# Kernel tuning notes

Measured on AMD Instinct MI355X. Metric: run time of the kernel, lower is better.

The kernel has to match this reference:

```python
import jax, jax.numpy as jnp
import numpy as np

B, S, D = 4, 4096, 1024
E, K, H = 8, 2, 2048


def setup_inputs() -> dict:
    key = jax.random.key(0)
    ks = jax.random.split(key, 6)
    scale_g = 1.0 / np.sqrt(D)
    scale_1 = 1.0 / np.sqrt(D)
    scale_2 = 1.0 / np.sqrt(H)
    return {
        "x": jax.random.normal(ks[0], (B, S, D), dtype=jnp.float32),
        "Wg": jax.random.uniform(ks[1], (D, E), jnp.float32, -scale_g, scale_g),
        "W1": jax.random.uniform(ks[2], (E, D, H), jnp.float32, -scale_1, scale_1),
        "b1": jax.random.uniform(ks[3], (E, H), jnp.float32, -scale_1, scale_1),
        "W2": jax.random.uniform(ks[4], (E, H, D), jnp.float32, -scale_2, scale_2),
        "b2": jax.random.uniform(ks[5], (E, D), jnp.float32, -scale_2, scale_2),
    }


def reference(x, Wg, W1, b1, W2, b2):
    # Router: softmax gate, top-k selection, renormalized combine weights
    logits = jnp.einsum("bsd,de->bse", x, Wg)          # [B,S,E]
    probs = jax.nn.softmax(logits, axis=-1)
    topv, topi = jax.lax.top_k(probs, K)                # [B,S,K]
    cw = topv / (jnp.sum(topv, axis=-1, keepdims=True) + 1e-9)
    # Per-token weight for each expert: sum over k of one_hot(idx_k)*cw_k -> [B,S,E]
    we = jnp.sum(jax.nn.one_hot(topi, E, dtype=x.dtype) * cw[..., None], axis=-2)
    # Weighted combine of per-expert FFN outputs (loop over small fixed E)
    y = jnp.zeros_like(x)
    for e in range(E):
        h = jax.nn.relu(jnp.einsum("bsd,dh->bsh", x, W1[e]) + b1[e])
        out_e = jnp.einsum("bsh,hd->bsd", h, W2[e]) + b2[e]
        y = y + we[..., e:e + 1] * out_e
    return y
```

## Files before the change

kernel.cpp:

```cpp
#include <hip/hip_runtime.h>
#include <hip/hip_bf16.h>

#define TOK 16384
#define DIM 1024
#define HID 2048
#define NEXP 8

typedef __attribute__((ext_vector_type(4))) float f32x4;
typedef __attribute__((ext_vector_type(8))) short s16x8;

__device__ __forceinline__ unsigned short f2bf(float f) {
  union { float f; unsigned u; } v; v.f = f;
  unsigned r = v.u + 0x7fffu + ((v.u >> 16) & 1u);
  return (unsigned short)(r >> 16);
}
__device__ __forceinline__ int tile_byte(int r, int kk2) {
  return (r * 128 + kk2) ^ ((r & 7) << 4);
}
__device__ __forceinline__ void gld_lds16(const void* g, void* l) {
  __builtin_amdgcn_global_load_lds(
      (const __attribute__((address_space(1))) unsigned int*)g,
      (__attribute__((address_space(3))) unsigned int*)l, 16, 0, 0);
}

__global__ void x_cvt(const float* __restrict__ x, unsigned short* __restrict__ xbf) {
  size_t i = ((size_t)blockIdx.x * blockDim.x + threadIdx.x) * 8;
  float4 a = *(const float4*)(x + i);
  float4 b = *(const float4*)(x + i + 4);
  s16x8 v;
  v[0] = (short)f2bf(a.x); v[1] = (short)f2bf(a.y);
  v[2] = (short)f2bf(a.z); v[3] = (short)f2bf(a.w);
  v[4] = (short)f2bf(b.x); v[5] = (short)f2bf(b.y);
  v[6] = (short)f2bf(b.z); v[7] = (short)f2bf(b.w);
  *(s16x8*)(xbf + i) = v;
}

__global__ void wg_tr(const float* __restrict__ Wg, float* __restrict__ WgT) {
  int i = blockIdx.x * 256 + threadIdx.x;
  int e = i >> 10, dd = i & 1023;
  WgT[i] = Wg[dd * NEXP + e];
}

__global__ void prep_tiles(const float* __restrict__ src, unsigned short* __restrict__ dst,
                           int rows, int cols) {
  int ct = blockIdx.x, kb = blockIdx.y, e = blockIdx.z;
  int nct = gridDim.x, nkb = gridDim.y;
  __shared__ __align__(16) unsigned short tile[8192];
  const float* s = src + ((size_t)e * rows + kb * 64) * cols + ct * 128;
  int tid = threadIdx.x;
  #pragma unroll
  for (int it = 0; it < 8; it++) {
    int idx = it * 256 + tid;
    int kk = idx >> 5;
    int r4 = (idx & 31) * 4;
    float4 v = *(const float4*)(s + (size_t)kk * cols + r4);
    char* tb = (char*)tile;
    *(unsigned short*)(tb + tile_byte(r4 + 0, kk * 2)) = f2bf(v.x);
    *(unsigned short*)(tb + tile_byte(r4 + 1, kk * 2)) = f2bf(v.y);
    *(unsigned short*)(tb + tile_byte(r4 + 2, kk * 2)) = f2bf(v.z);
    *(unsigned short*)(tb + tile_byte(r4 + 3, kk * 2)) = f2bf(v.w);
  }
  __syncthreads();
  unsigned short* d = dst + (((size_t)e * nct + ct) * nkb + kb) * 8192;
  #pragma unroll
  for (int it = 0; it < 4; it++) {
    int o = it * 256 + tid;
    *(s16x8*)(d + o * 8) = *(const s16x8*)((const char*)tile + o * 16);
  }
}

__global__ __launch_bounds__(256)
void router_logits(const float* __restrict__ x, const float* __restrict__ WgT,
                   int* __restrict__ sel, float2* __restrict__ wp) {
  int wave = threadIdx.x >> 6, lane = threadIdx.x & 63;
  int t = blockIdx.x * 4 + wave;
  const f32x4* xr = (const f32x4*)(x + (size_t)t * DIM);
  float acc[NEXP];
  #pragma unroll
  for (int e = 0; e < NEXP; e++) acc[e] = 0.f;
  #pragma unroll
  for (int q = 0; q < 4; q++) {
    f32x4 xv = xr[q * 64 + lane];
    #pragma unroll
    for (int e = 0; e < NEXP; e++) {
      f32x4 wv = *(const f32x4*)(WgT + (size_t)e * DIM + (q * 64 + lane) * 4);
      acc[e] = fmaf(xv[3], wv[3], fmaf(xv[2], wv[2], fmaf(xv[1], wv[1], fmaf(xv[0], wv[0], acc[e]))));
    }
  }
  #pragma unroll
  for (int e = 0; e < NEXP; e++) {
    float v = acc[e];
    #pragma unroll
    for (int off = 32; off >= 1; off >>= 1) v += __shfl_xor(v, off);
    acc[e] = v;
  }
  if (lane == 0) {
    float m = acc[0];
    #pragma unroll
    for (int e = 1; e < NEXP; e++) m = fmaxf(m, acc[e]);
    float p[NEXP], s = 0.f;
    #pragma unroll
    for (int e = 0; e < NEXP; e++) { p[e] = expf(acc[e] - m); s += p[e]; }
    float inv = 1.f / s;
    int i0 = 0; float v0 = p[0];
    #pragma unroll
    for (int e = 1; e < NEXP; e++) if (p[e] > v0) { v0 = p[e]; i0 = e; }
    int i1 = -1; float v1 = -1.f;
    #pragma unroll
    for (int e = 0; e < NEXP; e++) if (e != i0 && p[e] > v1) { v1 = p[e]; i1 = e; }
    v0 *= inv; v1 *= inv;
    float den = v0 + v1 + 1e-9f;
    sel[t] = i0 | (i1 << 4);
    wp[t] = make_float2(v0 / den, v1 / den);
  }
}

__global__ __launch_bounds__(256)
void router_scatter(const int* __restrict__ sel, const float2* __restrict__ wp,
                    int* __restrict__ counts, int* __restrict__ tok_list,
                    float* __restrict__ w_list) {
  __shared__ int lh0[4][16], lh1[4][16];
  __shared__ int bbase[16];
  int tid = threadIdx.x, wave = tid >> 6, lane = tid & 63;
  int t = blockIdx.x * 256 + tid;
  int s = sel[t];
  int b0 = s & 15;
  int b1 = 8 + ((s >> 4) & 15);
  float2 w = wp[t];
  unsigned long long lt = (lane == 63) ? ~0ull >> 1 : (((unsigned long long)1 << lane) - 1);
  int r0 = 0, r1 = 0;
  #pragma unroll
  for (int b = 0; b < 8; b++) {
    unsigned long long m0 = __ballot(b0 == b);
    if (b0 == b) r0 = __popcll(m0 & lt);
    if (lane == 0) { lh0[wave][b] = __popcll(m0); lh1[wave][b] = 0; }
  }
  #pragma unroll
  for (int b = 8; b < 16; b++) {
    unsigned long long m1 = __ballot(b1 == b);
    if (b1 == b) r1 = __popcll(m1 & lt);
    if (lane == 0) { lh1[wave][b] = __popcll(m1); lh0[wave][b] = 0; }
  }
  __syncthreads();
  if (tid < 16) {
    int h = 0;
    #pragma unroll
    for (int v = 0; v < 4; v++) h += lh0[v][tid] + lh1[v][tid];
    bbase[tid] = atomicAdd(&counts[tid], h);
  }
  __syncthreads();
  int p0 = bbase[b0] + r0;
  int p1 = bbase[b1] + r1;
  #pragma unroll
  for (int v = 0; v < 4; v++) {
    if (v < wave) { p0 += lh0[v][b0]; p1 += lh1[v][b1]; }
  }
  int e0 = b0, e1 = b1 - 8;
  tok_list[e0 * TOK + p0] = t;
  w_list[e0 * TOK + p0] = w.x;
  int q1 = TOK - 1 - p1;
  tok_list[e1 * TOK + q1] = t;
  w_list[e1 * TOK + q1] = w.y;
}

__global__ void calc_off(const int* __restrict__ counts, int* __restrict__ off) {
  if (threadIdx.x == 0 && blockIdx.x == 0) {
    int a = 0;
    for (int e = 0; e < NEXP; e++)
      for (int s = 0; s < 2; s++) {
        off[e * 2 + s] = a;
        a += (counts[s * 8 + e] + 127) & ~127;
      }
  }
}

__global__ __launch_bounds__(256, 4)
void moe_gemm1(const unsigned short* __restrict__ xbf, const unsigned short* __restrict__ w1s,
               const float* __restrict__ b1, const int* __restrict__ counts,
               const int* __restrict__ off, const int* __restrict__ tok_list,
               unsigned short* __restrict__ h_s, int ct_off, int nkbc) {
  int g = blockIdx.x;
  int e = -1, seg = 0, rt = 0, segcnt = 0, base = 0;
  #pragma unroll
  for (int zz = 0; zz < 16; zz++) {
    int ee = zz >> 1, ss = zz & 1;
    int c = counts[ss * 8 + ee];
    int nt = (c + 127) >> 7;
    if (e < 0 && g < base + nt) { e = ee; seg = ss; rt = g - base; segcnt = c; }
    base += nt;
  }
  if (e < 0) return;

  __shared__ __align__(16) unsigned short As[8192];
  __shared__ __align__(16) unsigned short Bs[8192];
  __shared__ int tokS[128];

  int tid = threadIdx.x, wave = tid >> 6, lane = tid & 63;
  int llo = lane & 15, lhi = lane >> 4;
  int wr = wave >> 1, wc = wave & 1;
  int ct_g = ct_off + blockIdx.y;

  if (tid < 128) {
    int q = rt * 128 + tid;
    int qq = q < segcnt ? q : segcnt - 1;
    int slot = seg ? (TOK - 1 - qq) : qq;
    tokS[tid] = tok_list[e * TOK + slot];
  }
  __syncthreads();

  const char* srcA[4];
  #pragma unroll
  for (int i = 0; i < 4; i++) {
    int r = i * 32 + (tid >> 3);
    srcA[i] = (const char*)xbf + (size_t)tokS[r] * (DIM * 2) + (((tid & 7) ^ (r & 7)) * 16);
  }
  const char* gB = (const char*)(w1s + (((size_t)e * 16 + ct_g) * 16) * 8192);

  f32x4 acc[4][4];
  #pragma unroll
  for (int i = 0; i < 4; i++)
    #pragma unroll
    for (int j = 0; j < 4; j++) acc[i][j] = (f32x4){0.f, 0.f, 0.f, 0.f};

  for (int kb = 0; kb < 16; kb++) {
    #pragma unroll
    for (int i = 0; i < 4; i++)
      gld_lds16(srcA[i] + kb * 128, (char*)As + i * 4096 + wave * 1024);
    const char* gs = gB + (size_t)kb * 16384 + wave * 1024 + lane * 16;
    #pragma unroll
    for (int i = 0; i < 4; i++)
      gld_lds16(gs + i * 4096, (char*)Bs + i * 4096 + wave * 1024);
    __syncthreads();
    #pragma unroll
    for (int ks = 0; ks < 2; ks++) {
      s16x8 a[4], b[4];
      #pragma unroll
      for (int f = 0; f < 4; f++) {
        a[f] = *(const s16x8*)((const char*)As + tile_byte(wr * 64 + f * 16 + llo, ks * 64 + lhi * 16));
        b[f] = *(const s16x8*)((const char*)Bs + tile_byte(wc * 64 + f * 16 + llo, ks * 64 + lhi * 16));
      }
      #pragma unroll
      for (int fr = 0; fr < 4; fr++)
        #pragma unroll
        for (int fc = 0; fc < 4; fc++)
          acc[fr][fc] = __builtin_amdgcn_mfma_f32_16x16x32_bf16(a[fr], b[fc], acc[fr][fc], 0, 0, 0);
    }
    __syncthreads();
  }

  size_t grt = (size_t)(off[e * 2 + seg] >> 7) + rt;
  unsigned short* hb = h_s + grt * ((size_t)nkbc * 8192);
  const float* b1e = b1 + e * HID + ct_g * 128;
  #pragma unroll
  for (int fc = 0; fc < 4; fc++) {
    int col = wc * 64 + fc * 16 + llo;
    float bv = b1e[col];
    char* tb = (char*)(hb + ((size_t)(blockIdx.y * 2 + (col >> 6))) * 8192);
    int kk2 = (col & 63) * 2;
    #pragma unroll
    for (int fr = 0; fr < 4; fr++) {
      int r0 = wr * 64 + fr * 16 + lhi * 4;
      #pragma unroll
      for (int j = 0; j < 4; j++) {
        float v = fmaxf(acc[fr][fc][j] + bv, 0.f);
        *(unsigned short*)(tb + tile_byte(r0 + j, kk2)) = f2bf(v);
      }
    }
  }
}

template<int NKBC>
__global__ __launch_bounds__(256, 4)
void moe_gemm2(const unsigned short* __restrict__ h_s, const unsigned short* __restrict__ w2s,
               const float* __restrict__ b2, const int* __restrict__ counts,
               const int* __restrict__ off, const int* __restrict__ tok_list,
               const float* __restrict__ w_list, float* __restrict__ y,
               int seg, int kb_off, int add_b2, int accum) {
  int g = blockIdx.x, ct = blockIdx.y;
  int e = -1, rt = 0, segcnt = 0, base = 0;
  #pragma unroll
  for (int ee = 0; ee < 8; ee++) {
    int c = counts[seg * 8 + ee];
    int nt = (c + 127) >> 7;
    if (e < 0 && g < base + nt) { e = ee; rt = g - base; segcnt = c; }
    base += nt;
  }
  if (e < 0) return;

  __shared__ __align__(16) unsigned short As[8192];
  __shared__ __align__(16) unsigned short Bs[8192];

  int tid = threadIdx.x, wave = tid >> 6, lane = tid & 63;
  int llo = lane & 15, lhi = lane >> 4;
  int wr = wave >> 1, wc = wave & 1;

  size_t grt = (size_t)(off[e * 2 + seg] >> 7) + rt;
  const char* gA = (const char*)(h_s + grt * ((size_t)NKBC * 8192));
  const char* gB = (const char*)(w2s + (((size_t)e * 8 + ct) * 32 + kb_off) * 8192);

  f32x4 acc[4][4];
  #pragma unroll
  for (int i = 0; i < 4; i++)
    #pragma unroll
    for (int j = 0; j < 4; j++) acc[i][j] = (f32x4){0.f, 0.f, 0.f, 0.f};

  for (int kb = 0; kb < NKBC; kb++) {
    const char* ga = gA + (size_t)kb * 16384 + wave * 1024 + lane * 16;
    const char* gb = gB + (size_t)kb * 16384 + wave * 1024 + lane * 16;
    #pragma unroll
    for (int i = 0; i < 4; i++) {
      gld_lds16(ga + i * 4096, (char*)As + i * 4096 + wave * 1024);
      gld_lds16(gb + i * 4096, (char*)Bs + i * 4096 + wave * 1024);
    }
    __syncthreads();
    #pragma unroll
    for (int ks = 0; ks < 2; ks++) {
      s16x8 a[4], b[4];
      #pragma unroll
      for (int f = 0; f < 4; f++) {
        a[f] = *(const s16x8*)((const char*)As + tile_byte(wr * 64 + f * 16 + llo, ks * 64 + lhi * 16));
        b[f] = *(const s16x8*)((const char*)Bs + tile_byte(wc * 64 + f * 16 + llo, ks * 64 + lhi * 16));
      }
      #pragma unroll
      for (int fr = 0; fr < 4; fr++)
        #pragma unroll
        for (int fc = 0; fc < 4; fc++)
          acc[fr][fc] = __builtin_amdgcn_mfma_f32_16x16x32_bf16(a[fr], b[fc], acc[fr][fc], 0, 0, 0);
    }
    __syncthreads();
  }

  const float* b2e = b2 + e * DIM + ct * 128;
  #pragma unroll
  for (int fr = 0; fr < 4; fr++) {
    #pragma unroll
    for (int j = 0; j < 4; j++) {
      int q = rt * 128 + wr * 64 + fr * 16 + lhi * 4 + j;
      if (q < segcnt) {
        int slot = seg ? (TOK - 1 - q) : q;
        int t = tok_list[e * TOK + slot];
        float w = w_list[e * TOK + slot];
        float bs = add_b2 ? w : 0.f;
        #pragma unroll
        for (int fc = 0; fc < 4; fc++) {
          int col = wc * 64 + fc * 16 + llo;
          float val = w * acc[fr][fc][j] + bs * b2e[col];
          size_t idx = (size_t)t * DIM + ct * 128 + col;
          if (accum) y[idx] += val;
          else       y[idx] = val;
        }
      }
    }
  }
}

__global__ void transpose_cvt(const float* __restrict__ src, unsigned short* __restrict__ dst,
                              int R, int C) {
  __shared__ float tile[32][33];
  int e = blockIdx.z;
  const float* s = src + (size_t)e * R * C;
  unsigned short* d = dst + (size_t)e * R * C;
  int c0 = blockIdx.x * 32, r0 = blockIdx.y * 32;
  int tx = threadIdx.x, ty = threadIdx.y;
  #pragma unroll
  for (int i = 0; i < 32; i += 8)
    tile[ty + i][tx] = s[(size_t)(r0 + ty + i) * C + c0 + tx];
  __syncthreads();
  #pragma unroll
  for (int i = 0; i < 32; i += 8)
    d[(size_t)(c0 + ty + i) * R + r0 + tx] = f2bf(tile[tx][ty + i]);
}

__global__ void router_kernel(const float* __restrict__ x, const float* __restrict__ Wg,
                              int* __restrict__ counts, int* __restrict__ tok_list,
                              float* __restrict__ w_list) {
  int wave = threadIdx.x >> 6, lane = threadIdx.x & 63;
  int t = blockIdx.x * 4 + wave;
  const float* xr = x + (size_t)t * DIM;
  float acc[NEXP];
  #pragma unroll
  for (int e = 0; e < NEXP; e++) acc[e] = 0.f;
  for (int i = 0; i < DIM / 64; i++) {
    int dd = i * 64 + lane;
    float xv = xr[dd];
    const float* wr = Wg + (size_t)dd * NEXP;
    #pragma unroll
    for (int e = 0; e < NEXP; e++) acc[e] = fmaf(xv, wr[e], acc[e]);
  }
  #pragma unroll
  for (int e = 0; e < NEXP; e++) {
    float v = acc[e];
    #pragma unroll
    for (int off = 32; off >= 1; off >>= 1) v += __shfl_xor(v, off);
    acc[e] = v;
  }
  if (lane == 0) {
    float m = acc[0];
    #pragma unroll
    for (int e = 1; e < NEXP; e++) m = fmaxf(m, acc[e]);
    float p[NEXP], s = 0.f;
    #pragma unroll
    for (int e = 0; e < NEXP; e++) { p[e] = expf(acc[e] - m); s += p[e]; }
    float inv = 1.f / s;
    int i0 = 0; float v0 = p[0];
    #pragma unroll
    for (int e = 1; e < NEXP; e++) if (p[e] > v0) { v0 = p[e]; i0 = e; }
    int i1 = -1; float v1 = -1.f;
    #pragma unroll
    for (int e = 0; e < NEXP; e++) if (e != i0 && p[e] > v1) { v1 = p[e]; i1 = e; }
    v0 *= inv; v1 *= inv;
    float den = v0 + v1 + 1e-9f;
    float w0 = v0 / den, w1 = v1 / den;
    int q0 = atomicAdd(&counts[i0], 1);
    tok_list[i0 * TOK + q0] = t;           w_list[i0 * TOK + q0] = w0;
    int q1 = atomicAdd(&counts[8 + i1], 1);
    int p1 = TOK - 1 - q1;
    tok_list[i1 * TOK + p1] = t;           w_list[i1 * TOK + p1] = w1;
  }
}

__global__ __launch_bounds__(512, 4)
void moe_ffn_kernel(const float* __restrict__ x,
                    const unsigned short* __restrict__ w1t,
                    const unsigned short* __restrict__ w2t,
                    const float* __restrict__ b1, const float* __restrict__ b2,
                    const int* __restrict__ counts, const int* __restrict__ tok_list,
                    const float* __restrict__ w_list, float* __restrict__ y) {
  int zz = blockIdx.y, e = zz & 7, seg = zz >> 3;
  int segcnt = counts[seg * 8 + e];
  int row0 = blockIdx.x * 32;
  if (row0 >= segcnt) return;
  __shared__ unsigned short Xs[32 * DIM];
  __shared__ unsigned short hsl[32 * 64];
  __shared__ int tokS[32];
  __shared__ float wS[32];
  int tid = threadIdx.x, wave = tid >> 6, lane = tid & 63;
  if (tid < 32) {
    int q = row0 + tid;
    if (q < segcnt) {
      int slot = seg ? (TOK - 1 - q) : q;
      tokS[tid] = tok_list[e * TOK + slot]; wS[tid] = w_list[e * TOK + slot];
    } else { tokS[tid] = -1; wS[tid] = 0.f; }
  }
  __syncthreads();
  #pragma unroll
  for (int it = 0; it < 8; it++) {
    int chunk = it * 512 + tid;
    int r = chunk >> 7, c = (chunk & 127) * 8;
    int tok = tokS[r];
    float4 f0 = make_float4(0.f, 0.f, 0.f, 0.f), f1 = f0;
    if (tok >= 0) {
      const float4* xp = (const float4*)(x + (size_t)tok * DIM + c);
      f0 = xp[0]; f1 = xp[1];
    }
    s16x8 bv;
    bv[0] = (short)f2bf(f0.x); bv[1] = (short)f2bf(f0.y);
    bv[2] = (short)f2bf(f0.z); bv[3] = (short)f2bf(f0.w);
    bv[4] = (short)f2bf(f1.x); bv[5] = (short)f2bf(f1.y);
    bv[6] = (short)f2bf(f1.z); bv[7] = (short)f2bf(f1.w);
    int byte = (r * DIM + c) * 2; byte ^= (r & 7) << 4;
    *(s16x8*)((char*)Xs + byte) = bv;
  }
  __syncthreads();
  int rw = wave >> 2, cw = wave & 3;
  int lhi = lane >> 4, llo = lane & 15;
  f32x4 acc[16];
  #pragma unroll
  for (int i = 0; i < 16; i++) acc[i] = (f32x4){0.f, 0.f, 0.f, 0.f};
  int arow = rw * 16 + llo;
  int abase = arow * (DIM * 2) + lhi * 16;
  int aswz = (arow & 7) << 4;
  int h_abase = arow * (64 * 2) + lhi * 16;
  const size_t eHD = (size_t)e * HID * DIM;
  const unsigned short* w2e = w2t + (size_t)e * DIM * HID;
  for (int hc = 0; hc < HID; hc += 64) {
    f32x4 c1 = (f32x4){0.f, 0.f, 0.f, 0.f};
    const unsigned short* w1p = w1t + eHD + (size_t)(hc + cw * 16 + llo) * DIM + lhi * 8;
    #pragma unroll 4
    for (int k = 0; k < DIM; k += 32) {
      s16x8 a = *(const s16x8*)((const char*)Xs + ((abase + k * 2) ^ aswz));
      s16x8 b = *(const s16x8*)(w1p + k);
      c1 = __builtin_amdgcn_mfma_f32_16x16x32_bf16(a, b, c1, 0, 0, 0);
    }
    float b1v = b1[e * HID + hc + cw * 16 + llo];
    __syncthreads();
    #pragma unroll
    for (int j = 0; j < 4; j++) {
      int r = rw * 16 + lhi * 4 + j;
      float v = fmaxf(c1[j] + b1v, 0.f);
      int byte = (r * 64 + cw * 16 + llo) * 2; byte ^= (r & 7) << 4;
      *(unsigned short*)((char*)hsl + byte) = f2bf(v);
    }
    __syncthreads();
    s16x8 a0 = *(const s16x8*)((const char*)hsl + ((h_abase + 0)  ^ aswz));
    s16x8 a1 = *(const s16x8*)((const char*)hsl + ((h_abase + 64) ^ aswz));
    const unsigned short* w2p0 = w2e + hc + lhi * 8;
    #pragma unroll 4
    for (int ctile = 0; ctile < 16; ctile++) {
      int dcol = cw * 256 + ctile * 16 + llo;
      const unsigned short* bp = w2p0 + (size_t)dcol * HID;
      s16x8 b0 = *(const s16x8*)(bp);
      s16x8 b1f = *(const s16x8*)(bp + 32);
      acc[ctile] = __builtin_amdgcn_mfma_f32_16x16x32_bf16(a0, b0, acc[ctile], 0, 0, 0);
      acc[ctile] = __builtin_amdgcn_mfma_f32_16x16x32_bf16(a1, b1f, acc[ctile], 0, 0, 0);
    }
  }
  const float* b2e = b2 + e * DIM;
  #pragma unroll
  for (int ctile = 0; ctile < 16; ctile++) {
    int dcol = cw * 256 + ctile * 16 + llo;
    float b2v = b2e[dcol];
    #pragma unroll
    for (int j = 0; j < 4; j++) {
      int r = rw * 16 + lhi * 4 + j;
      int tok = tokS[r];
      if (tok >= 0) atomicAdd(&y[(size_t)tok * DIM + dcol], wS[r] * (acc[ctile][j] + b2v));
    }
  }
}

extern "C" void kernel_launch(void* const* d_in, const int* in_sizes, int n_in,
                              void* d_out, int out_size, void* d_ws, size_t ws_size,
                              hipStream_t stream) {
  const float* x  = (const float*)d_in[0];
  const float* Wg = (const float*)d_in[1];
  const float* W1 = (const float*)d_in[2];
  const float* b1 = (const float*)d_in[3];
  const float* W2 = (const float*)d_in[4];
  const float* b2 = (const float*)d_in[5];
  float* y = (float*)d_out;
  char* ws = (char*)d_ws;

  const size_t O_COUNTS = 0;
  const size_t O_OFF    = 1024;
  const size_t O_TOK    = 2048;
  const size_t O_W      = O_TOK + (size_t)NEXP * TOK * 4;
  const size_t O_WGT    = O_W + (size_t)NEXP * TOK * 4;
  const size_t O_SEL    = O_WGT + (size_t)NEXP * DIM * 4;
  const size_t O_WP     = O_SEL + (size_t)TOK * 4;
  const size_t O_W1S    = O_WP + (size_t)TOK * 8;
  const size_t O_W2S    = O_W1S + (size_t)NEXP * 16 * 16 * 8192 * 2;
  const size_t O_XBF    = O_W2S + (size_t)NEXP * 8 * 32 * 8192 * 2;
  const size_t O_HS     = O_XBF + (size_t)TOK * DIM * 2;

  int Hc = 0;
  if (ws_size > O_HS) {
    size_t avail = ws_size - O_HS;
    for (int hc = HID; hc >= 128; hc >>= 1)
      if ((size_t)34816 * hc * 2 <= avail) { Hc = hc; break; }
  }

  if (Hc) {
    int*   counts   = (int*)(ws + O_COUNTS);
    int*   offp     = (int*)(ws + O_OFF);
    int*   tok_list = (int*)(ws + O_TOK);
    float* w_list   = (float*)(ws + O_W);
    float* WgT      = (float*)(ws + O_WGT);
    int*   sel      = (int*)(ws + O_SEL);
    float2* wp      = (float2*)(ws + O_WP);
    unsigned short* w1s = (unsigned short*)(ws + O_W1S);
    unsigned short* w2s = (unsigned short*)(ws + O_W2S);
    unsigned short* xbf = (unsigned short*)(ws + O_XBF);
    unsigned short* hs  = (unsigned short*)(ws + O_HS);

    hipMemsetAsync(counts, 0, 2048, stream);
    wg_tr<<<32, 256, 0, stream>>>(Wg, WgT);
    x_cvt<<<TOK * DIM / 8 / 256, 256, 0, stream>>>(x, xbf);
    prep_tiles<<<dim3(HID / 128, DIM / 64, NEXP), 256, 0, stream>>>(W1, w1s, DIM, HID);
    prep_tiles<<<dim3(DIM / 128, HID / 64, NEXP), 256, 0, stream>>>(W2, w2s, HID, DIM);
    router_logits<<<TOK / 4, 256, 0, stream>>>(x, WgT, sel, wp);
    router_scatter<<<TOK / 256, 256, 0, stream>>>(sel, wp, counts, tok_list, w_list);
    calc_off<<<1, 64, 0, stream>>>(counts, offp);

    int nch = HID / Hc, nkbc = Hc / 64, nct = Hc / 128;
    for (int ch = 0; ch < nch; ch++) {
      moe_gemm1<<<dim3(272, nct), 256, 0, stream>>>(
          xbf, w1s, b1, counts, offp, tok_list, hs, ch * nct, nkbc);
      for (int seg = 0; seg < 2; seg++) {
        int add_b2 = (ch == 0) ? 1 : 0;
        int accum  = (ch == 0 && seg == 0) ? 0 : 1;
        int kb_off = ch * nkbc;
        #define LG2(NK) moe_gemm2<NK><<<dim3(136, 8), 256, 0, stream>>>( \
            hs, w2s, b2, counts, offp, tok_list, w_list, y, seg, kb_off, add_b2, accum)
        switch (nkbc) {
          case 32: LG2(32); break;
          case 16: LG2(16); break;
          case 8:  LG2(8);  break;
          case 4:  LG2(4);  break;
          default: LG2(2);  break;
        }
        #undef LG2
      }
    }
  } else {
    int*   counts   = (int*)ws;
    int*   tok_list = (int*)(ws + 2048);
    float* w_list   = (float*)(ws + 2048 + (size_t)NEXP * TOK * 4);
    unsigned short* w1t = (unsigned short*)(ws + 2048 + (size_t)NEXP * TOK * 8);
    unsigned short* w2t = w1t + (size_t)NEXP * HID * DIM;

    hipMemsetAsync(d_out, 0, (size_t)out_size * sizeof(float), stream);
    hipMemsetAsync(counts, 0, 2048, stream);
    transpose_cvt<<<dim3(HID / 32, DIM / 32, NEXP), dim3(32, 8), 0, stream>>>(W1, w1t, DIM, HID);
    transpose_cvt<<<dim3(DIM / 32, HID / 32, NEXP), dim3(32, 8), 0, stream>>>(W2, w2t, HID, DIM);
    router_kernel<<<TOK / 4, 256, 0, stream>>>(x, Wg, counts, tok_list, w_list);
    moe_ffn_kernel<<<dim3(TOK / 32, 16), 512, 0, stream>>>(
        x, w1t, w2t, b1, b2, counts, tok_list, w_list, y);
  }
}
```

Measured before the change: 591.5 us.

## Fuse x bf16 conversion into router and XCD-swizzle MoE GEMM block order

```diff
diff --git a/kernel.cpp b/kernel.cpp
--- a/kernel.cpp
+++ b/kernel.cpp
@@ -22,17 +22,10 @@
       (const __attribute__((address_space(1))) unsigned int*)g,
       (__attribute__((address_space(3))) unsigned int*)l, 16, 0, 0);
 }
-
-__global__ void x_cvt(const float* __restrict__ x, unsigned short* __restrict__ xbf) {
-  size_t i = ((size_t)blockIdx.x * blockDim.x + threadIdx.x) * 8;
-  float4 a = *(const float4*)(x + i);
-  float4 b = *(const float4*)(x + i + 4);
-  s16x8 v;
-  v[0] = (short)f2bf(a.x); v[1] = (short)f2bf(a.y);
-  v[2] = (short)f2bf(a.z); v[3] = (short)f2bf(a.w);
-  v[4] = (short)f2bf(b.x); v[5] = (short)f2bf(b.y);
-  v[6] = (short)f2bf(b.z); v[7] = (short)f2bf(b.w);
-  *(s16x8*)(xbf + i) = v;
+__device__ __forceinline__ int xcd_swz(int p, int nwg) {
+  int q = nwg >> 3, r = nwg & 7;
+  int xcd = p & 7, idx = p >> 3;
+  return (xcd < r ? xcd * (q + 1) : r * (q + 1) + (xcd - r) * q) + idx;
 }
 
 __global__ void wg_tr(const float* __restrict__ Wg, float* __restrict__ WgT) {
@@ -70,17 +63,22 @@
 }
 
 __global__ __launch_bounds__(256)
-void router_logits(const float* __restrict__ x, const float* __restrict__ WgT,
-                   int* __restrict__ sel, float2* __restrict__ wp) {
+void router_logits_cvt(const float* __restrict__ x, const float* __restrict__ WgT,
+                       unsigned short* __restrict__ xbf,
+                       int* __restrict__ sel, float2* __restrict__ wp) {
   int wave = threadIdx.x >> 6, lane = threadIdx.x & 63;
   int t = blockIdx.x * 4 + wave;
   const f32x4* xr = (const f32x4*)(x + (size_t)t * DIM);
+  unsigned short* xb = xbf + (size_t)t * DIM;
   float acc[NEXP];
   #pragma unroll
   for (int e = 0; e < NEXP; e++) acc[e] = 0.f;
   #pragma unroll
   for (int q = 0; q < 4; q++) {
     f32x4 xv = xr[q * 64 + lane];
+    ushort4 bv;
+    bv.x = f2bf(xv[0]); bv.y = f2bf(xv[1]); bv.z = f2bf(xv[2]); bv.w = f2bf(xv[3]);
+    *(ushort4*)(xb + (q * 64 + lane) * 4) = bv;
     #pragma unroll
     for (int e = 0; e < NEXP; e++) {
       f32x4 wv = *(const f32x4*)(WgT + (size_t)e * DIM + (q * 64 + lane) * 4);
@@ -178,8 +176,10 @@
 void moe_gemm1(const unsigned short* __restrict__ xbf, const unsigned short* __restrict__ w1s,
                const float* __restrict__ b1, const int* __restrict__ counts,
                const int* __restrict__ off, const int* __restrict__ tok_list,
-               unsigned short* __restrict__ h_s, int ct_off, int nkbc) {
-  int g = blockIdx.x;
+               unsigned short* __restrict__ h_s, int ct_off, int nkbc, int nct) {
+  int logical = xcd_swz(blockIdx.x, gridDim.x);
+  int ct_l = logical % nct;
+  int g = logical / nct;
   int e = -1, seg = 0, rt = 0, segcnt = 0, base = 0;
   #pragma unroll
   for (int zz = 0; zz < 16; zz++) {
@@ -198,7 +198,7 @@
   int tid = threadIdx.x, wave = tid >> 6, lane = tid & 63;
   int llo = lane & 15, lhi = lane >> 4;
   int wr = wave >> 1, wc = wave & 1;
-  int ct_g = ct_off + blockIdx.y;
+  int ct_g = ct_off + ct_l;
 
   if (tid < 128) {
     int q = rt * 128 + tid;
@@ -255,7 +255,7 @@
   for (int fc = 0; fc < 4; fc++) {
     int col = wc * 64 + fc * 16 + llo;
     float bv = b1e[col];
-    char* tb = (char*)(hb + ((size_t)(blockIdx.y * 2 + (col >> 6))) * 8192);
+    char* tb = (char*)(hb + ((size_t)(ct_l * 2 + (col >> 6))) * 8192);
     int kk2 = (col & 63) * 2;
     #pragma unroll
     for (int fr = 0; fr < 4; fr++) {
@@ -276,7 +276,9 @@
                const int* __restrict__ off, const int* __restrict__ tok_list,
                const float* __restrict__ w_list, float* __restrict__ y,
                int seg, int kb_off, int add_b2, int accum) {
-  int g = blockIdx.x, ct = blockIdx.y;
+  int logical = xcd_swz(blockIdx.x, gridDim.x);
+  int ct = logical & 7;
+  int g = logical >> 3;
   int e = -1, rt = 0, segcnt = 0, base = 0;
   #pragma unroll
   for (int ee = 0; ee < 8; ee++) {
@@ -565,22 +567,21 @@
 
     hipMemsetAsync(counts, 0, 2048, stream);
     wg_tr<<<32, 256, 0, stream>>>(Wg, WgT);
-    x_cvt<<<TOK * DIM / 8 / 256, 256, 0, stream>>>(x, xbf);
     prep_tiles<<<dim3(HID / 128, DIM / 64, NEXP), 256, 0, stream>>>(W1, w1s, DIM, HID);
     prep_tiles<<<dim3(DIM / 128, HID / 64, NEXP), 256, 0, stream>>>(W2, w2s, HID, DIM);
-    router_logits<<<TOK / 4, 256, 0, stream>>>(x, WgT, sel, wp);
+    router_logits_cvt<<<TOK / 4, 256, 0, stream>>>(x, WgT, xbf, sel, wp);
     router_scatter<<<TOK / 256, 256, 0, stream>>>(sel, wp, counts, tok_list, w_list);
     calc_off<<<1, 64, 0, stream>>>(counts, offp);
 
     int nch = HID / Hc, nkbc = Hc / 64, nct = Hc / 128;
     for (int ch = 0; ch < nch; ch++) {
-      moe_gemm1<<<dim3(272, nct), 256, 0, stream>>>(
-          xbf, w1s, b1, counts, offp, tok_list, hs, ch * nct, nkbc);
+      moe_gemm1<<<272 * nct, 256, 0, stream>>>(
+          xbf, w1s, b1, counts, offp, tok_list, hs, ch * nct, nkbc, nct);
       for (int seg = 0; seg < 2; seg++) {
         int add_b2 = (ch == 0) ? 1 : 0;
         int accum  = (ch == 0 && seg == 0) ? 0 : 1;
         int kb_off = ch * nkbc;
-        #define LG2(NK) moe_gemm2<NK><<<dim3(136, 8), 256, 0, stream>>>( \
+        #define LG2(NK) moe_gemm2<NK><<<136 * 8, 256, 0, stream>>>( \
             hs, w2s, b2, counts, offp, tok_list, w_list, y, seg, kb_off, add_b2, accum)
         switch (nkbc) {
           case 32: LG2(32); break;
```

Result: faster. 513.4 us (-13.2%).
